# Performance work log

Measured on AMD Instinct MI355X. Metric: run time of the kernel, lower is better.

## Reference

```python
import jax, jax.numpy as jnp
import numpy as np

N = 20000      # nodes
E = 320000     # edges per metapath graph
M = 3          # metapaths
IN = 256       # input feat dim
HID = 64       # num_hidden per head
NH = 4         # nhead (layer 1)
OUT = 256      # out_dim
NHO = 1        # nhead_out (layer 2)
SA_H = 128     # semantic attention hidden
NEG_SLOPE = 0.2


def gat_conv(h, W, attn_l, attn_r, src, dst, apply_relu):
    # h: [N, F_in]; W: [F_in, H*D]; attn_l/attn_r: [H, D]
    H, D = attn_l.shape
    feat = (h @ W).reshape(N, H, D)                      # [N, H, D]
    el = jnp.sum(feat * attn_l, axis=-1)                 # [N, H]
    er = jnp.sum(feat * attn_r, axis=-1)                 # [N, H]
    e = jax.nn.leaky_relu(el[src] + er[dst], NEG_SLOPE)  # [E, H]
    # edge softmax grouped by destination node
    emax = jax.ops.segment_max(e, dst, num_segments=N)   # [N, H] (-inf for empty)
    emax = jnp.where(jnp.isfinite(emax), emax, 0.0)
    ee = jnp.exp(e - emax[dst])                          # [E, H]
    denom = jax.ops.segment_sum(ee, dst, num_segments=N) # [N, H]
    alpha = ee / (denom[dst] + 1e-9)                     # [E, H]
    msg = alpha[:, :, None] * feat[src]                  # [E, H, D]
    out = jax.ops.segment_sum(msg, dst, num_segments=N)  # [N, H, D]
    out = out.reshape(N, H * D)                          # concat heads
    return jax.nn.relu(out) if apply_relu else out


def semantic_attention(z, W1, b1, v):
    # z: [N, M, F]
    w = jnp.tanh(z @ W1 + b1) @ v          # [N, M, 1]
    w = w.mean(axis=0)                     # [M, 1]
    beta = jax.nn.softmax(w, axis=0)       # [M, 1]
    out = jnp.sum(beta[None, :, :] * z, axis=1)  # [N, F]
    att_mp = beta.squeeze()                # [M]
    return out, att_mp


def setup_inputs() -> dict:
    key = jax.random.key(0)
    ks = jax.random.split(key, 16)
    s = 0.05
    return {
        "x": jax.random.normal(ks[0], (N, IN), dtype=jnp.float32),
        "edges": jax.random.randint(ks[1], (M, 2, E), 0, N, dtype=jnp.int64)
                 if jax.config.jax_enable_x64 else
                 jax.random.randint(ks[1], (M, 2, E), 0, N, dtype=jnp.int32),
        "W1": jax.random.normal(ks[2], (IN, NH * HID), dtype=jnp.float32) * s,
        "al1": jax.random.normal(ks[3], (NH, HID), dtype=jnp.float32) * s,
        "ar1": jax.random.normal(ks[4], (NH, HID), dtype=jnp.float32) * s,
        "saW1": jax.random.normal(ks[5], (NH * HID, SA_H), dtype=jnp.float32) * s,
        "sab1": jnp.zeros((SA_H,), dtype=jnp.float32),
        "sav1": jax.random.normal(ks[6], (SA_H, 1), dtype=jnp.float32) * s,
        "W2": jax.random.normal(ks[7], (NH * HID, NHO * OUT), dtype=jnp.float32) * s,
        "al2": jax.random.normal(ks[8], (NHO, OUT), dtype=jnp.float32) * s,
        "ar2": jax.random.normal(ks[9], (NHO, OUT), dtype=jnp.float32) * s,
        "saW2": jax.random.normal(ks[10], (NHO * OUT, SA_H), dtype=jnp.float32) * s,
        "sab2": jnp.zeros((SA_H,), dtype=jnp.float32),
        "sav2": jax.random.normal(ks[11], (SA_H, 1), dtype=jnp.float32) * s,
    }


def reference(x, edges, W1, al1, ar1, saW1, sab1, sav1,
              W2, al2, ar2, saW2, sab2, sav2):
    h = x
    # HAN layer 1: shared GATConv over each metapath graph, relu activation
    z = jnp.stack([gat_conv(h, W1, al1, ar1, edges[i, 0], edges[i, 1], True)
                   for i in range(M)], axis=1)          # [N, M, NH*HID]
    h, att_mp = semantic_attention(z, saW1, sab1, sav1)
    # HAN layer 2: last layer, no activation (encoding=False)
    z = jnp.stack([gat_conv(h, W2, al2, ar2, edges[i, 0], edges[i, 1], False)
                   for i in range(M)], axis=1)          # [N, M, NHO*OUT]
    h, att_mp = semantic_attention(z, saW2, sab2, sav2)
    return h, att_mp
```

## Files before the change

kernel.cpp:

```cpp
#include <hip/hip_runtime.h>
#include <hip/hip_bf16.h>
#include <math.h>

#define NN 20000
#define EE 320000
#define MM 3
#define FW 256
#define SAH 128
#define NB 79

static __device__ __forceinline__ float lrelu(float x){ return x > 0.f ? x : 0.2f*x; }

static __device__ __forceinline__ unsigned short f2bf(float f) {
    unsigned u = __float_as_uint(f);
    return (unsigned short)((u + 0x7FFFu + ((u >> 16) & 1u)) >> 16);
}
static __device__ __forceinline__ float bf2f(unsigned short b) {
    return __uint_as_float(((unsigned)b) << 16);
}
static __device__ __forceinline__ float bflo(unsigned u){ return __uint_as_float(u << 16); }
static __device__ __forceinline__ float bfhi(unsigned u){ return __uint_as_float(u & 0xffff0000u); }
static __device__ __forceinline__ unsigned pk2bf(float lo, float hi) {
    return ((unsigned)f2bf(lo)) | (((unsigned)f2bf(hi)) << 16);
}

__global__ __launch_bounds__(256) void hist_kernel(const int* __restrict__ edges, int* __restrict__ cnt) {
    int idx = blockIdx.x*256 + threadIdx.x;
    if (idx >= MM*EE) return;
    int m = idx / EE, e = idx - m*EE;
    int dst = edges[(m*2+1)*EE + e];
    atomicAdd(&cnt[m*NN + dst], 1);
}

__global__ __launch_bounds__(256) void scanA_kernel(const int* __restrict__ cnt, int* __restrict__ rowptr, int* __restrict__ bsum) {
    int m = blockIdx.y;
    int i = blockIdx.x*256 + threadIdx.x;
    int v = (i < NN) ? cnt[m*NN + i] : 0;
    int lane = threadIdx.x & 63;
    int val = v;
    #pragma unroll
    for (int o = 1; o < 64; o <<= 1) { int t = __shfl_up(val, o); if (lane >= o) val += t; }
    __shared__ int ws[4];
    int w = threadIdx.x >> 6;
    if (lane == 63) ws[w] = val;
    __syncthreads();
    #pragma unroll
    for (int j = 0; j < 3; ++j) if (j < w) val += ws[j];
    if (i < NN) rowptr[m*(NN+1) + 1 + i] = val;
    if (threadIdx.x == 255) bsum[m*NB + blockIdx.x] = val;
}

__global__ __launch_bounds__(128) void scanB_kernel(const int* __restrict__ bsum, int* __restrict__ boff) {
    __shared__ int s[128];
    int t = threadIdx.x;
    for (int m = 0; m < MM; ++m) {
        int v = (t < NB) ? bsum[m*NB + t] : 0;
        s[t] = v; __syncthreads();
        for (int o = 1; o < 128; o <<= 1) {
            int x = (t >= o) ? s[t - o] : 0;
            __syncthreads();
            s[t] += x;
            __syncthreads();
        }
        if (t < NB) boff[m*NB + t] = s[t] - v;
        __syncthreads();
    }
}

__global__ __launch_bounds__(256) void scanC_kernel(const int* __restrict__ cnt, int* __restrict__ rowptr,
                                                    const int* __restrict__ boff, int* __restrict__ cursor) {
    int m = blockIdx.y;
    int i = blockIdx.x*256 + threadIdx.x;
    if (i >= NN) return;
    int incl = rowptr[m*(NN+1) + 1 + i] + boff[m*NB + blockIdx.x];
    rowptr[m*(NN+1) + 1 + i] = incl;
    cursor[m*NN + i] = incl - cnt[m*NN + i];
    if (i == 0 && blockIdx.x == 0) rowptr[m*(NN+1)] = 0;
}

__global__ __launch_bounds__(256) void scatter_kernel(const int* __restrict__ edges, int* __restrict__ cursor,
                                                      int* __restrict__ csr_src, int* __restrict__ csr_dst) {
    int idx = blockIdx.x*256 + threadIdx.x;
    if (idx >= MM*EE) return;
    int m = idx / EE, e = idx - m*EE;
    int src = edges[m*2*EE + e];
    int dst = edges[(m*2+1)*EE + e];
    int pos = atomicAdd(&cursor[m*NN + dst], 1);
    csr_src[m*EE + pos] = src;
    csr_dst[m*EE + pos] = dst;
}

template<int H>
__global__ __launch_bounds__(256) void gemm_attn_kernel(const float* __restrict__ A, const float* __restrict__ B,
                                                        const float* __restrict__ attl, const float* __restrict__ attr,
                                                        unsigned short* __restrict__ C, float* __restrict__ el,
                                                        float* __restrict__ er, int Mrows) {
    __shared__ float As[16][68];
    __shared__ float Bs[16][68];
    int tid = threadIdx.x;
    int tx = tid & 15, ty = tid >> 4;
    int row0 = blockIdx.x*64, col0 = blockIdx.y*64;
    float c[4][4] = {};
    int arow = row0 + (tid >> 2);
    int arl  = tid >> 2;
    int ak   = (tid & 3) * 4;
    int bkr  = tid >> 4, bcc = (tid & 15) * 4;

    for (int k0 = 0; k0 < 256; k0 += 16) {
        float4 av = make_float4(0.f,0.f,0.f,0.f);
        if (arow < Mrows) av = *(const float4*)&A[(size_t)arow*256 + k0 + ak];
        As[ak+0][arl] = av.x; As[ak+1][arl] = av.y; As[ak+2][arl] = av.z; As[ak+3][arl] = av.w;
        float4 bv = *(const float4*)&B[(size_t)(k0 + bkr)*256 + col0 + bcc];
        *(float4*)&Bs[bkr][bcc] = bv;
        __syncthreads();
        #pragma unroll
        for (int k = 0; k < 16; ++k) {
            float4 a = *(float4*)&As[k][ty*4];
            float4 b = *(float4*)&Bs[k][tx*4];
            c[0][0] += a.x*b.x; c[0][1] += a.x*b.y; c[0][2] += a.x*b.z; c[0][3] += a.x*b.w;
            c[1][0] += a.y*b.x; c[1][1] += a.y*b.y; c[1][2] += a.y*b.z; c[1][3] += a.y*b.w;
            c[2][0] += a.z*b.x; c[2][1] += a.z*b.y; c[2][2] += a.z*b.z; c[2][3] += a.z*b.w;
            c[3][0] += a.w*b.x; c[3][1] += a.w*b.y; c[3][2] += a.w*b.z; c[3][3] += a.w*b.w;
        }
        __syncthreads();
    }

    float alv[4], arv[4];
    #pragma unroll
    for (int j = 0; j < 4; ++j) { alv[j] = attl[col0 + tx*4 + j]; arv[j] = attr[col0 + tx*4 + j]; }
    int h = (H == 4) ? (int)blockIdx.y : 0;
    #pragma unroll
    for (int i = 0; i < 4; ++i) {
        int r = row0 + ty*4 + i;
        float pel = c[i][0]*alv[0] + c[i][1]*alv[1] + c[i][2]*alv[2] + c[i][3]*alv[3];
        float per = c[i][0]*arv[0] + c[i][1]*arv[1] + c[i][2]*arv[2] + c[i][3]*arv[3];
        #pragma unroll
        for (int o = 1; o < 16; o <<= 1) { pel += __shfl_xor(pel, o); per += __shfl_xor(per, o); }
        if (r < Mrows) {
            ushort4 cv;
            cv.x = f2bf(c[i][0]); cv.y = f2bf(c[i][1]); cv.z = f2bf(c[i][2]); cv.w = f2bf(c[i][3]);
            *(ushort4*)&C[(size_t)r*256 + col0 + tx*4] = cv;
            if (tx == 0) { atomicAdd(&el[r*H + h], pel); atomicAdd(&er[r*H + h], per); }
        }
    }
}

template<int H>
__global__ __launch_bounds__(256) void edge_ee_kernel(const int* __restrict__ csr_src, const int* __restrict__ csr_dst,
                                                      const float* __restrict__ el, const float* __restrict__ er,
                                                      float* __restrict__ ee) {
    int idx = blockIdx.x*256 + threadIdx.x;
    if (idx >= MM*EE) return;
    int src = csr_src[idx], dst = csr_dst[idx];
    if (H == 4) {
        float4 l = *(const float4*)&el[src*4];
        float4 r = *(const float4*)&er[dst*4];
        float4 s;
        s.x = expf(lrelu(l.x + r.x));
        s.y = expf(lrelu(l.y + r.y));
        s.z = expf(lrelu(l.z + r.z));
        s.w = expf(lrelu(l.w + r.w));
        *(float4*)&ee[(size_t)idx*4] = s;
    } else {
        ee[idx] = expf(lrelu(el[src] + er[dst]));
    }
}

template<int H, bool RELU>
__global__ __launch_bounds__(256) void agg_kernel(const unsigned short* __restrict__ feat,
                                                  const float* __restrict__ ee,
                                                  const int* __restrict__ rowptr,
                                                  const int* __restrict__ csr_src,
                                                  unsigned short* __restrict__ z) {
    int m = blockIdx.y;
    int tid = threadIdx.x;
    int lane = tid & 63, wv = tid >> 6;
    int n = blockIdx.x * 4 + wv;
    int eslot = lane >> 5, flane = lane & 31;
    int h = (H == 4) ? (flane >> 3) : 0;
    int beg = rowptr[m*(NN+1) + n], end = rowptr[m*(NN+1) + n + 1];
    const int eb = m*EE;

    float a[8] = {};
    float den = 0.f;
    int e0 = beg + eslot;

    int   sA = 0, sB = 0;
    float wA = 0.f, wB = 0.f;
    if (e0 < end)     { sA = csr_src[eb+e0];   wA = (H==4)? ee[(size_t)(eb+e0  )*4+h] : ee[eb+e0  ]; }
    if (e0 + 2 < end) { sB = csr_src[eb+e0+2]; wB = (H==4)? ee[(size_t)(eb+e0+2)*4+h] : ee[eb+e0+2]; }

    for (int e = e0; e < end; e += 2) {
        uint4 v = *(const uint4*)(feat + (size_t)sA*256 + flane*8);
        float w = wA;
        sA = sB; wA = wB;
        if (e + 4 < end) {
            sB = csr_src[eb+e+4];
            wB = (H==4)? ee[(size_t)(eb+e+4)*4+h] : ee[eb+e+4];
        }
        den += w;
        a[0] += w * bflo(v.x); a[1] += w * bfhi(v.x);
        a[2] += w * bflo(v.y); a[3] += w * bfhi(v.y);
        a[4] += w * bflo(v.z); a[5] += w * bfhi(v.z);
        a[6] += w * bflo(v.w); a[7] += w * bfhi(v.w);
    }

    #pragma unroll
    for (int j = 0; j < 8; ++j) a[j] += __shfl_xor(a[j], 32);
    den += __shfl_xor(den, 32);

    if (eslot == 0) {
        float inv = 1.f / (den + 1e-9f);
        #pragma unroll
        for (int j = 0; j < 8; ++j) {
            a[j] *= inv;
            if (RELU) a[j] = fmaxf(a[j], 0.f);
        }
        uint4 pk;
        pk.x = pk2bf(a[0], a[1]);
        pk.y = pk2bf(a[2], a[3]);
        pk.z = pk2bf(a[4], a[5]);
        pk.w = pk2bf(a[6], a[7]);
        *(uint4*)&z[((size_t)n*MM + m)*256 + flane*8] = pk;
    }
}

__global__ __launch_bounds__(256) void semw_kernel(const unsigned short* __restrict__ Z, const float* __restrict__ W,
                                                   const float* __restrict__ bias, const float* __restrict__ v,
                                                   float* __restrict__ wsum) {
    __shared__ float As[16][68];
    __shared__ float Bs[16][132];
    int tid = threadIdx.x;
    int tx = tid & 31, ty = tid >> 5;
    int row0 = blockIdx.x * 64;
    float c[8][4] = {};
    int arl = tid >> 2, arow = row0 + arl, ak = (tid & 3)*4;
    int bkr = tid >> 4, bcc = (tid & 15) * 8;

    for (int k0 = 0; k0 < 256; k0 += 16) {
        float4 av = make_float4(0.f,0.f,0.f,0.f);
        if (arow < NN*MM) {
            uint2 zv = *(const uint2*)&Z[(size_t)arow*256 + k0 + ak];
            av.x = bflo(zv.x); av.y = bfhi(zv.x); av.z = bflo(zv.y); av.w = bfhi(zv.y);
        }
        As[ak+0][arl] = av.x; As[ak+1][arl] = av.y; As[ak+2][arl] = av.z; As[ak+3][arl] = av.w;
        float4 b0 = *(const float4*)&W[(size_t)(k0 + bkr)*SAH + bcc];
        float4 b1 = *(const float4*)&W[(size_t)(k0 + bkr)*SAH + bcc + 4];
        *(float4*)&Bs[bkr][bcc]     = b0;
        *(float4*)&Bs[bkr][bcc + 4] = b1;
        __syncthreads();
        #pragma unroll
        for (int k = 0; k < 16; ++k) {
            float4 a0 = *(float4*)&As[k][ty*8];
            float4 a1 = *(float4*)&As[k][ty*8 + 4];
            float4 b  = *(float4*)&Bs[k][tx*4];
            float aa[8] = {a0.x,a0.y,a0.z,a0.w,a1.x,a1.y,a1.z,a1.w};
            #pragma unroll
            for (int i = 0; i < 8; ++i) {
                c[i][0] += aa[i]*b.x; c[i][1] += aa[i]*b.y; c[i][2] += aa[i]*b.z; c[i][3] += aa[i]*b.w;
            }
        }
        __syncthreads();
    }

    float bb[4], vv[4];
    #pragma unroll
    for (int j = 0; j < 4; ++j) { bb[j] = bias[tx*4 + j]; vv[j] = v[tx*4 + j]; }

    float loc[3] = {0.f, 0.f, 0.f};
    #pragma unroll
    for (int i = 0; i < 8; ++i) {
        int row = row0 + ty*8 + i;
        float p = tanhf(c[i][0] + bb[0]) * vv[0] + tanhf(c[i][1] + bb[1]) * vv[1]
                + tanhf(c[i][2] + bb[2]) * vv[2] + tanhf(c[i][3] + bb[3]) * vv[3];
        #pragma unroll
        for (int o = 1; o < 32; o <<= 1) p += __shfl_xor(p, o);
        if (tx == 0 && row < NN*MM) loc[row % MM] += p;
    }
    __shared__ float red[8][3];
    if (tx == 0) { red[ty][0] = loc[0]; red[ty][1] = loc[1]; red[ty][2] = loc[2]; }
    __syncthreads();
    if (tid < MM) {
        float s = 0.f;
        #pragma unroll
        for (int j = 0; j < 8; ++j) s += red[j][tid];
        atomicAdd(&wsum[tid], s);
    }
}

__global__ void beta_kernel(const float* __restrict__ wsum, float* __restrict__ beta, float* att_out) {
    if (threadIdx.x == 0 && blockIdx.x == 0) {
        float w0 = wsum[0] / (float)NN, w1 = wsum[1] / (float)NN, w2 = wsum[2] / (float)NN;
        float mx = fmaxf(w0, fmaxf(w1, w2));
        float e0 = expf(w0 - mx), e1 = expf(w1 - mx), e2 = expf(w2 - mx);
        float s = e0 + e1 + e2;
        beta[0] = e0 / s; beta[1] = e1 / s; beta[2] = e2 / s;
        if (att_out) { att_out[0] = e0/s; att_out[1] = e1/s; att_out[2] = e2/s; }
    }
}

__global__ __launch_bounds__(128) void combine_kernel(const unsigned short* __restrict__ z, const float* __restrict__ beta,
                                                      float* __restrict__ out) {
    int n = blockIdx.x, t = threadIdx.x;
    float b0 = beta[0], b1 = beta[1], b2 = beta[2];
    size_t base = (size_t)n*MM*256 + t*2;
    unsigned z0 = *(const unsigned*)&z[base];
    unsigned z1 = *(const unsigned*)&z[base + 256];
    unsigned z2 = *(const unsigned*)&z[base + 512];
    float2 o;
    o.x = b0*bflo(z0) + b1*bflo(z1) + b2*bflo(z2);
    o.y = b0*bfhi(z0) + b1*bfhi(z1) + b2*bfhi(z2);
    *(float2*)&out[(size_t)n*256 + t*2] = o;
}

extern "C" void kernel_launch(void* const* d_in, const int* in_sizes, int n_in,
                              void* d_out, int out_size, void* d_ws, size_t ws_size,
                              hipStream_t stream) {
    const float* x    = (const float*)d_in[0];
    const int*   edges= (const int*)  d_in[1];
    const float* W1   = (const float*)d_in[2];
    const float* al1  = (const float*)d_in[3];
    const float* ar1  = (const float*)d_in[4];
    const float* saW1 = (const float*)d_in[5];
    const float* sab1 = (const float*)d_in[6];
    const float* sav1 = (const float*)d_in[7];
    const float* W2   = (const float*)d_in[8];
    const float* al2  = (const float*)d_in[9];
    const float* ar2  = (const float*)d_in[10];
    const float* saW2 = (const float*)d_in[11];
    const float* sab2 = (const float*)d_in[12];
    const float* sav2 = (const float*)d_in[13];
    float* out = (float*)d_out;

    char* ws = (char*)d_ws;
    size_t off = 0;
    auto alloc = [&](size_t bytes) { void* p = ws + off; off += (bytes + 255) & ~(size_t)255; return p; };
    unsigned short* feat = (unsigned short*)alloc((size_t)NN*256*2);
    unsigned short* z    = (unsigned short*)alloc((size_t)NN*MM*256*2);
    float* ee     = (float*)alloc((size_t)MM*EE*4*4);
    float* el     = (float*)alloc(NN*4*4);
    float* er     = (float*)alloc(NN*4*4);
    float* wsum   = (float*)alloc(256);
    float* beta   = (float*)alloc(256);
    int*   cnt    = (int*)alloc(MM*NN*4);
    int*   cursor = (int*)alloc(MM*NN*4);
    int*   rowptr = (int*)alloc(MM*(NN+1)*4);
    int*   csr_s  = (int*)alloc((size_t)MM*EE*4);
    int*   csr_d  = (int*)alloc((size_t)MM*EE*4);
    int*   bsum   = (int*)alloc(MM*NB*4);
    int*   boff   = (int*)alloc(MM*NB*4);
    float* h = out;

    int egrid = (MM*EE + 255)/256;
    dim3 sg(NB, MM);

    hipMemsetAsync(cnt, 0, MM*NN*4, stream);
    hist_kernel<<<egrid, 256, 0, stream>>>(edges, cnt);
    scanA_kernel<<<sg, 256, 0, stream>>>(cnt, rowptr, bsum);
    scanB_kernel<<<1, 128, 0, stream>>>(bsum, boff);
    scanC_kernel<<<sg, 256, 0, stream>>>(cnt, rowptr, boff, cursor);
    scatter_kernel<<<egrid, 256, 0, stream>>>(edges, cursor, csr_s, csr_d);

    hipMemsetAsync(el, 0, NN*4*4, stream);
    hipMemsetAsync(er, 0, NN*4*4, stream);
    gemm_attn_kernel<4><<<dim3(313, 4), 256, 0, stream>>>(x, W1, al1, ar1, feat, el, er, NN);
    edge_ee_kernel<4><<<egrid, 256, 0, stream>>>(csr_s, csr_d, el, er, ee);
    agg_kernel<4, true><<<dim3(NN/4, MM), 256, 0, stream>>>(feat, ee, rowptr, csr_s, z);
    hipMemsetAsync(wsum, 0, 16, stream);
    semw_kernel<<<938, 256, 0, stream>>>(z, saW1, sab1, sav1, wsum);
    beta_kernel<<<1, 64, 0, stream>>>(wsum, beta, nullptr);
    combine_kernel<<<NN, 128, 0, stream>>>(z, beta, h);

    hipMemsetAsync(el, 0, NN*4, stream);
    hipMemsetAsync(er, 0, NN*4, stream);
    gemm_attn_kernel<1><<<dim3(313, 4), 256, 0, stream>>>(h, W2, al2, ar2, feat, el, er, NN);
    edge_ee_kernel<1><<<egrid, 256, 0, stream>>>(csr_s, csr_d, el, er, ee);
    agg_kernel<1, false><<<dim3(NN/4, MM), 256, 0, stream>>>(feat, ee, rowptr, csr_s, z);
    hipMemsetAsync(wsum, 0, 16, stream);
    semw_kernel<<<938, 256, 0, stream>>>(z, saW2, sab2, sav2, wsum);
    beta_kernel<<<1, 64, 0, stream>>>(wsum, beta, out + (size_t)NN*256);
    combine_kernel<<<NN, 128, 0, stream>>>(z, beta, out);
}
```

Before: 482.5 us.

## Replace FP32 SIMT GEMMs with bf16 MFMA kernels using pre-transposed weights

A prep kernel converts x to bf16 and transposes all weight matrices into bf16. The projection GEMM and the semantic-attention GEMM are rewritten to use 16x16x32 bf16 MFMA instructions, with operands loaded straight from global memory into registers. The layer-1 combine now writes bf16 into the layer-2 GEMM input. el/er are written directly, which drops the atomics and the memsets. This removes the slow FP32 FMA GEMMs at the cost of extra bf16 rounding of x and the weights, plus one additional conversion pass over x.

```diff
diff --git a/kernel.cpp b/kernel.cpp
--- a/kernel.cpp
+++ b/kernel.cpp
@@ -9,19 +9,43 @@
 #define SAH 128
 #define NB 79
 
+typedef __attribute__((ext_vector_type(8))) short bf16x8;
+typedef __attribute__((ext_vector_type(4))) float f32x4;
+
 static __device__ __forceinline__ float lrelu(float x){ return x > 0.f ? x : 0.2f*x; }
 
 static __device__ __forceinline__ unsigned short f2bf(float f) {
     unsigned u = __float_as_uint(f);
     return (unsigned short)((u + 0x7FFFu + ((u >> 16) & 1u)) >> 16);
-}
-static __device__ __forceinline__ float bf2f(unsigned short b) {
-    return __uint_as_float(((unsigned)b) << 16);
 }
 static __device__ __forceinline__ float bflo(unsigned u){ return __uint_as_float(u << 16); }
 static __device__ __forceinline__ float bfhi(unsigned u){ return __uint_as_float(u & 0xffff0000u); }
 static __device__ __forceinline__ unsigned pk2bf(float lo, float hi) {
     return ((unsigned)f2bf(lo)) | (((unsigned)f2bf(hi)) << 16);
+}
+
+#define XBLK 2500
+__global__ __launch_bounds__(256) void prep_kernel(const float* __restrict__ x, unsigned short* __restrict__ xb,
+                                                   const float* __restrict__ W1, unsigned short* __restrict__ W1t,
+                                                   const float* __restrict__ saW1, unsigned short* __restrict__ saW1t,
+                                                   const float* __restrict__ W2, unsigned short* __restrict__ W2t,
+                                                   const float* __restrict__ saW2, unsigned short* __restrict__ saW2t) {
+    int b = blockIdx.x, tid = threadIdx.x;
+    if (b < XBLK) {
+        int i = b*256 + tid;
+        const float4* p = (const float4*)x + (size_t)i*2;
+        float4 v0 = p[0], v1 = p[1];
+        uint4 o;
+        o.x = pk2bf(v0.x, v0.y); o.y = pk2bf(v0.z, v0.w);
+        o.z = pk2bf(v1.x, v1.y); o.w = pk2bf(v1.z, v1.w);
+        ((uint4*)xb)[i] = o;
+        return;
+    }
+    int b2 = b - XBLK;
+    if (b2 < 256)      { int n = b2;       W1t  [(size_t)n*256 + tid] = f2bf(W1  [(size_t)tid*256 + n]); }
+    else if (b2 < 384) { int n = b2 - 256; saW1t[(size_t)n*256 + tid] = f2bf(saW1[(size_t)tid*SAH + n]); }
+    else if (b2 < 640) { int n = b2 - 384; W2t  [(size_t)n*256 + tid] = f2bf(W2  [(size_t)tid*256 + n]); }
+    else               { int n = b2 - 640; saW2t[(size_t)n*256 + tid] = f2bf(saW2[(size_t)tid*SAH + n]); }
 }
 
 __global__ __launch_bounds__(256) void hist_kernel(const int* __restrict__ edges, int* __restrict__ cnt) {
@@ -91,56 +115,88 @@
 }
 
 template<int H>
-__global__ __launch_bounds__(256) void gemm_attn_kernel(const float* __restrict__ A, const float* __restrict__ B,
+__global__ __launch_bounds__(256) void gemm_mfma_kernel(const unsigned short* __restrict__ A,
+                                                        const unsigned short* __restrict__ Bt,
                                                         const float* __restrict__ attl, const float* __restrict__ attr,
-                                                        unsigned short* __restrict__ C, float* __restrict__ el,
-                                                        float* __restrict__ er, int Mrows) {
-    __shared__ float As[16][68];
-    __shared__ float Bs[16][68];
+                                                        unsigned short* __restrict__ C,
+                                                        float* __restrict__ el, float* __restrict__ er) {
     int tid = threadIdx.x;
-    int tx = tid & 15, ty = tid >> 4;
-    int row0 = blockIdx.x*64, col0 = blockIdx.y*64;
-    float c[4][4] = {};
-    int arow = row0 + (tid >> 2);
-    int arl  = tid >> 2;
-    int ak   = (tid & 3) * 4;
-    int bkr  = tid >> 4, bcc = (tid & 15) * 4;
-
-    for (int k0 = 0; k0 < 256; k0 += 16) {
-        float4 av = make_float4(0.f,0.f,0.f,0.f);
-        if (arow < Mrows) av = *(const float4*)&A[(size_t)arow*256 + k0 + ak];
-        As[ak+0][arl] = av.x; As[ak+1][arl] = av.y; As[ak+2][arl] = av.z; As[ak+3][arl] = av.w;
-        float4 bv = *(const float4*)&B[(size_t)(k0 + bkr)*256 + col0 + bcc];
-        *(float4*)&Bs[bkr][bcc] = bv;
+    int w = tid >> 6, lane = tid & 63;
+    int rowgrp = w & 1, half = w >> 1;
+    int r0 = blockIdx.x*32 + rowgrp*16;
+    int colbase = half * 128;
+    int lrow = lane & 15, lk = lane >> 4;
+
+    bf16x8 a[8];
+    const unsigned short* ap = A + (size_t)(r0 + lrow)*256 + lk*8;
+    #pragma unroll
+    for (int k = 0; k < 8; ++k) a[k] = *(const bf16x8*)(ap + k*32);
+
+    float pelv[2][4] = {{0.f,0.f,0.f,0.f},{0.f,0.f,0.f,0.f}};
+    float perv[2][4] = {{0.f,0.f,0.f,0.f},{0.f,0.f,0.f,0.f}};
+
+    #pragma unroll
+    for (int n = 0; n < 8; ++n) {
+        int col0 = colbase + n*16;
+        const unsigned short* bp = Bt + (size_t)(col0 + lrow)*256 + lk*8;
+        f32x4 acc = {0.f, 0.f, 0.f, 0.f};
+        #pragma unroll
+        for (int k = 0; k < 8; ++k) {
+            bf16x8 bfr = *(const bf16x8*)(bp + k*32);
+            acc = __builtin_amdgcn_mfma_f32_16x16x32_bf16(a[k], bfr, acc, 0, 0, 0);
+        }
+        int col = col0 + lrow;
+        float al = attl[col], ar = attr[col];
+        int hl = (H == 4) ? (n >> 2) : 0;
+        #pragma unroll
+        for (int r = 0; r < 4; ++r) {
+            float cv = acc[r];
+            pelv[hl][r] += cv * al;
+            perv[hl][r] += cv * ar;
+            C[(size_t)(r0 + lk*4 + r)*256 + col] = f2bf(cv);
+        }
+    }
+
+    int nhl = (H == 4) ? 2 : 1;
+    #pragma unroll
+    for (int hl = 0; hl < 2; ++hl) {
+        if (hl >= nhl) break;
+        #pragma unroll
+        for (int r = 0; r < 4; ++r) {
+            float pe = pelv[hl][r], pr = perv[hl][r];
+            #pragma unroll
+            for (int o = 1; o < 16; o <<= 1) { pe += __shfl_xor(pe, o); pr += __shfl_xor(pr, o); }
+            pelv[hl][r] = pe; perv[hl][r] = pr;
+        }
+    }
+
+    if (H == 4) {
+        if (lrow == 0) {
+            int row = r0 + lk*4;
+            #pragma unroll
+            for (int hl = 0; hl < 2; ++hl) {
+                int head = half*2 + hl;
+                #pragma unroll
+                for (int r = 0; r < 4; ++r) {
+                    el[(size_t)(row + r)*4 + head] = pelv[hl][r];
+                    er[(size_t)(row + r)*4 + head] = perv[hl][r];
+                }
+            }
+        }
+    } else {
+        __shared__ float elds[2][32], erds[2][32];
+        if (lrow == 0) {
+            int rib = rowgrp*16 + lk*4;
+            #pragma unroll
+            for (int r = 0; r < 4; ++r) {
+                elds[half][rib + r] = pelv[0][r];
+                erds[half][rib + r] = perv[0][r];
+            }
+        }
         __syncthreads();
-        #pragma unroll
-        for (int k = 0; k < 16; ++k) {
-            float4 a = *(float4*)&As[k][ty*4];
-            float4 b = *(float4*)&Bs[k][tx*4];
-            c[0][0] += a.x*b.x; c[0][1] += a.x*b.y; c[0][2] += a.x*b.z; c[0][3] += a.x*b.w;
-            c[1][0] += a.y*b.x; c[1][1] += a.y*b.y; c[1][2] += a.y*b.z; c[1][3] += a.y*b.w;
-            c[2][0] += a.z*b.x; c[2][1] += a.z*b.y; c[2][2] += a.z*b.z; c[2][3] += a.z*b.w;
-            c[3][0] += a.w*b.x; c[3][1] += a.w*b.y; c[3][2] += a.w*b.z; c[3][3] += a.w*b.w;
-        }
-        __syncthreads();
-    }
-
-    float alv[4], arv[4];
-    #pragma unroll
-    for (int j = 0; j < 4; ++j) { alv[j] = attl[col0 + tx*4 + j]; arv[j] = attr[col0 + tx*4 + j]; }
-    int h = (H == 4) ? (int)blockIdx.y : 0;
-    #pragma unroll
-    for (int i = 0; i < 4; ++i) {
-        int r = row0 + ty*4 + i;
-        float pel = c[i][0]*alv[0] + c[i][1]*alv[1] + c[i][2]*alv[2] + c[i][3]*alv[3];
-        float per = c[i][0]*arv[0] + c[i][1]*arv[1] + c[i][2]*arv[2] + c[i][3]*arv[3];
-        #pragma unroll
-        for (int o = 1; o < 16; o <<= 1) { pel += __shfl_xor(pel, o); per += __shfl_xor(per, o); }
-        if (r < Mrows) {
-            ushort4 cv;
-            cv.x = f2bf(c[i][0]); cv.y = f2bf(c[i][1]); cv.z = f2bf(c[i][2]); cv.w = f2bf(c[i][3]);
-            *(ushort4*)&C[(size_t)r*256 + col0 + tx*4] = cv;
-            if (tx == 0) { atomicAdd(&el[r*H + h], pel); atomicAdd(&er[r*H + h], per); }
+        if (tid < 32) {
+            el[blockIdx.x*32 + tid] = elds[0][tid] + elds[1][tid];
+            er[blockIdx.x*32 + tid] = erds[0][tid] + erds[1][tid];
         }
     }
 }
@@ -225,67 +281,57 @@
     }
 }
 
-__global__ __launch_bounds__(256) void semw_kernel(const unsigned short* __restrict__ Z, const float* __restrict__ W,
-                                                   const float* __restrict__ bias, const float* __restrict__ v,
-                                                   float* __restrict__ wsum) {
-    __shared__ float As[16][68];
-    __shared__ float Bs[16][132];
+__global__ __launch_bounds__(256) void semw_mfma_kernel(const unsigned short* __restrict__ Z,
+                                                        const unsigned short* __restrict__ Wt,
+                                                        const float* __restrict__ bias, const float* __restrict__ v,
+                                                        float* __restrict__ wsum) {
     int tid = threadIdx.x;
-    int tx = tid & 31, ty = tid >> 5;
-    int row0 = blockIdx.x * 64;
-    float c[8][4] = {};
-    int arl = tid >> 2, arow = row0 + arl, ak = (tid & 3)*4;
-    int bkr = tid >> 4, bcc = (tid & 15) * 8;
-
-    for (int k0 = 0; k0 < 256; k0 += 16) {
-        float4 av = make_float4(0.f,0.f,0.f,0.f);
-        if (arow < NN*MM) {
-            uint2 zv = *(const uint2*)&Z[(size_t)arow*256 + k0 + ak];
-            av.x = bflo(zv.x); av.y = bfhi(zv.x); av.z = bflo(zv.y); av.w = bfhi(zv.y);
-        }
-        As[ak+0][arl] = av.x; As[ak+1][arl] = av.y; As[ak+2][arl] = av.z; As[ak+3][arl] = av.w;
-        float4 b0 = *(const float4*)&W[(size_t)(k0 + bkr)*SAH + bcc];
-        float4 b1 = *(const float4*)&W[(size_t)(k0 + bkr)*SAH + bcc + 4];
-        *(float4*)&Bs[bkr][bcc]     = b0;
-        *(float4*)&Bs[bkr][bcc + 4] = b1;
-        __syncthreads();
-        #pragma unroll
-        for (int k = 0; k < 16; ++k) {
-            float4 a0 = *(float4*)&As[k][ty*8];
-            float4 a1 = *(float4*)&As[k][ty*8 + 4];
-            float4 b  = *(float4*)&Bs[k][tx*4];
-            float aa[8] = {a0.x,a0.y,a0.z,a0.w,a1.x,a1.y,a1.z,a1.w};
-            #pragma unroll
-            for (int i = 0; i < 8; ++i) {
-                c[i][0] += aa[i]*b.x; c[i][1] += aa[i]*b.y; c[i][2] += aa[i]*b.z; c[i][3] += aa[i]*b.w;
-            }
-        }
-        __syncthreads();
-    }
-
-    float bb[4], vv[4];
-    #pragma unroll
-    for (int j = 0; j < 4; ++j) { bb[j] = bias[tx*4 + j]; vv[j] = v[tx*4 + j]; }
-
-    float loc[3] = {0.f, 0.f, 0.f};
-    #pragma unroll
-    for (int i = 0; i < 8; ++i) {
-        int row = row0 + ty*8 + i;
-        float p = tanhf(c[i][0] + bb[0]) * vv[0] + tanhf(c[i][1] + bb[1]) * vv[1]
-                + tanhf(c[i][2] + bb[2]) * vv[2] + tanhf(c[i][3] + bb[3]) * vv[3];
-        #pragma unroll
-        for (int o = 1; o < 32; o <<= 1) p += __shfl_xor(p, o);
-        if (tx == 0 && row < NN*MM) loc[row % MM] += p;
-    }
-    __shared__ float red[8][3];
-    if (tx == 0) { red[ty][0] = loc[0]; red[ty][1] = loc[1]; red[ty][2] = loc[2]; }
+    int w = tid >> 6, lane = tid & 63;
+    int r0 = blockIdx.x*64 + w*16;
+    int lrow = lane & 15, lk = lane >> 4;
+
+    int arow = r0 + lrow;
+    if (arow >= NN*MM) arow = NN*MM - 1;
+    bf16x8 a[8];
+    const unsigned short* ap = Z + (size_t)arow*256 + lk*8;
+    #pragma unroll
+    for (int k = 0; k < 8; ++k) a[k] = *(const bf16x8*)(ap + k*32);
+
+    float p[4] = {0.f, 0.f, 0.f, 0.f};
+    #pragma unroll
+    for (int n = 0; n < 8; ++n) {
+        int col = n*16 + lrow;
+        const unsigned short* bp = Wt + (size_t)col*256 + lk*8;
+        f32x4 acc = {0.f, 0.f, 0.f, 0.f};
+        #pragma unroll
+        for (int k = 0; k < 8; ++k) {
+            bf16x8 bfr = *(const bf16x8*)(bp + k*32);
+            acc = __builtin_amdgcn_mfma_f32_16x16x32_bf16(a[k], bfr, acc, 0, 0, 0);
+        }
+        float bb = bias[col], vv = v[col];
+        #pragma unroll
+        for (int r = 0; r < 4; ++r)
+            p[r] += tanhf(acc[r] + bb) * vv;
+    }
+
+    #pragma unroll
+    for (int r = 0; r < 4; ++r) {
+        #pragma unroll
+        for (int o = 1; o < 16; o <<= 1) p[r] += __shfl_xor(p[r], o);
+    }
+
+    __shared__ float loc[3];
+    if (tid < 3) loc[tid] = 0.f;
     __syncthreads();
-    if (tid < MM) {
-        float s = 0.f;
-        #pragma unroll
-        for (int j = 0; j < 8; ++j) s += red[j][tid];
-        atomicAdd(&wsum[tid], s);
-    }
+    if (lrow == 0) {
+        #pragma unroll
+        for (int r = 0; r < 4; ++r) {
+            int row = r0 + lk*4 + r;
+            if (row < NN*MM) atomicAdd(&loc[row % MM], p[r]);
+        }
+    }
+    __syncthreads();
+    if (tid < 3) atomicAdd(&wsum[tid], loc[tid]);
 }
 
 __global__ void beta_kernel(const float* __restrict__ wsum, float* __restrict__ beta, float* att_out) {
@@ -297,6 +343,19 @@
         beta[0] = e0 / s; beta[1] = e1 / s; beta[2] = e2 / s;
         if (att_out) { att_out[0] = e0/s; att_out[1] = e1/s; att_out[2] = e2/s; }
     }
+}
+
+__global__ __launch_bounds__(128) void combine_bf16_kernel(const unsigned short* __restrict__ z, const float* __restrict__ beta,
+                                                           unsigned short* __restrict__ outb) {
+    int n = blockIdx.x, t = threadIdx.x;
+    float b0 = beta[0], b1 = beta[1], b2 = beta[2];
+    size_t base = (size_t)n*MM*256 + t*2;
+    unsigned z0 = *(const unsigned*)&z[base];
+    unsigned z1 = *(const unsigned*)&z[base + 256];
+    unsigned z2 = *(const unsigned*)&z[base + 512];
+    float ox = b0*bflo(z0) + b1*bflo(z1) + b2*bflo(z2);
+    float oy = b0*bfhi(z0) + b1*bfhi(z1) + b2*bfhi(z2);
+    *(unsigned*)&outb[(size_t)n*256 + t*2] = pk2bf(ox, oy);
 }
 
 __global__ __launch_bounds__(128) void combine_kernel(const unsigned short* __restrict__ z, const float* __restrict__ beta,
@@ -335,8 +394,13 @@
     char* ws = (char*)d_ws;
     size_t off = 0;
     auto alloc = [&](size_t bytes) { void* p = ws + off; off += (bytes + 255) & ~(size_t)255; return p; };
-    unsigned short* feat = (unsigned short*)alloc((size_t)NN*256*2);
-    unsigned short* z    = (unsigned short*)alloc((size_t)NN*MM*256*2);
+    unsigned short* feat  = (unsigned short*)alloc((size_t)NN*256*2);
+    unsigned short* z     = (unsigned short*)alloc((size_t)NN*MM*256*2);
+    unsigned short* xb    = (unsigned short*)alloc((size_t)NN*256*2);
+    unsigned short* W1t   = (unsigned short*)alloc(256*256*2);
+    unsigned short* saW1t = (unsigned short*)alloc(SAH*256*2);
+    unsigned short* W2t   = (unsigned short*)alloc(256*256*2);
+    unsigned short* saW2t = (unsigned short*)alloc(SAH*256*2);
     float* ee     = (float*)alloc((size_t)MM*EE*4*4);
     float* el     = (float*)alloc(NN*4*4);
     float* er     = (float*)alloc(NN*4*4);
@@ -349,10 +413,12 @@
     int*   csr_d  = (int*)alloc((size_t)MM*EE*4);
     int*   bsum   = (int*)alloc(MM*NB*4);
     int*   boff   = (int*)alloc(MM*NB*4);
-    float* h = out;
+    unsigned short* hb = xb;
 
     int egrid = (MM*EE + 255)/256;
     dim3 sg(NB, MM);
+
+    prep_kernel<<<XBLK + 768, 256, 0, stream>>>(x, xb, W1, W1t, saW1, saW1t, W2, W2t, saW2, saW2t);
 
     hipMemsetAsync(cnt, 0, MM*NN*4, stream);
     hist_kernel<<<egrid, 256, 0, stream>>>(edges, cnt);
@@ -361,23 +427,19 @@
     scanC_kernel<<<sg, 256, 0, stream>>>(cnt, rowptr, boff, cursor);
     scatter_kernel<<<egrid, 256, 0, stream>>>(edges, cursor, csr_s, csr_d);
 
-    hipMemsetAsync(el, 0, NN*4*4, stream);
-    hipMemsetAsync(er, 0, NN*4*4, stream);
-    gemm_attn_kernel<4><<<dim3(313, 4), 256, 0, stream>>>(x, W1, al1, ar1, feat, el, er, NN);
+    gemm_mfma_kernel<4><<<NN/32, 256, 0, stream>>>(xb, W1t, al1, ar1, feat, el, er);
     edge_ee_kernel<4><<<egrid, 256, 0, stream>>>(csr_s, csr_d, el, er, ee);
     agg_kernel<4, true><<<dim3(NN/4, MM), 256, 0, stream>>>(feat, ee, rowptr, csr_s, z);
     hipMemsetAsync(wsum, 0, 16, stream);
-    semw_kernel<<<938, 256, 0, stream>>>(z, saW1, sab1, sav1, wsum);
+    semw_mfma_kernel<<<(NN*MM + 63)/64, 256, 0, stream>>>(z, saW1t, sab1, sav1, wsum);
     beta_kernel<<<1, 64, 0, stream>>>(wsum, beta, nullptr);
-    combine_kernel<<<NN, 128, 0, stream>>>(z, beta, h);
-
-    hipMemsetAsync(el, 0, NN*4, stream);
-    hipMemsetAsync(er, 0, NN*4, stream);
-    gemm_attn_kernel<1><<<dim3(313, 4), 256, 0, stream>>>(h, W2, al2, ar2, feat, el, er, NN);
+    combine_bf16_kernel<<<NN, 128, 0, stream>>>(z, beta, hb);
+
+    gemm_mfma_kernel<1><<<NN/32, 256, 0, stream>>>(hb, W2t, al2, ar2, feat, el, er);
     edge_ee_kernel<1><<<egrid, 256, 0, stream>>>(csr_s, csr_d, el, er, ee);
     agg_kernel<1, false><<<dim3(NN/4, MM), 256, 0, stream>>>(feat, ee, rowptr, csr_s, z);
     hipMemsetAsync(wsum, 0, 16, stream);
-    semw_kernel<<<938, 256, 0, stream>>>(z, saW2, sab2, sav2, wsum);
+    semw_mfma_kernel<<<(NN*MM + 63)/64, 256, 0, stream>>>(z, saW2t, sab2, sav2, wsum);
     beta_kernel<<<1, 64, 0, stream>>>(wsum, beta, out + (size_t)NN*256);
     combine_kernel<<<NN, 128, 0, stream>>>(z, beta, out);
 }
```

After: 416.6 us. -13.7%, faster.
